# Optimization experiments

Hardware: AMD Instinct MI355X
Metric: run time of the kernel (lower is better)

Reference implementation:

```python
import jax, jax.numpy as jnp
import numpy as np

D = 1024
H = 16
HD = D // H
FF = 4 * D
EPS = 1e-5


def setup_inputs() -> dict:
    key = jax.random.key(0)
    ks = jax.random.split(key, 16)
    s = lambda k, shape, scale: jax.random.normal(k, shape, dtype=jnp.float32) * scale
    inp = {
        "x": s(ks[0], (8, 1024, D), 1.0),
        "Wq": s(ks[1], (D, D), D ** -0.5), "bq": jnp.zeros((D,), jnp.float32),
        "Wk": s(ks[2], (D, D), D ** -0.5), "bk": jnp.zeros((D,), jnp.float32),
        "Wv": s(ks[3], (D, D), D ** -0.5), "bv": jnp.zeros((D,), jnp.float32),
        "Wo": s(ks[4], (D, D), D ** -0.5), "bo": jnp.zeros((D,), jnp.float32),
        "W1": s(ks[5], (D, FF), D ** -0.5), "b1": jnp.zeros((FF,), jnp.float32),
        "W2": s(ks[6], (FF, D), FF ** -0.5), "b2": jnp.zeros((D,), jnp.float32),
        "g1": jnp.ones((D,), jnp.float32), "be1": jnp.zeros((D,), jnp.float32),
        "g2": jnp.ones((D,), jnp.float32), "be2": jnp.zeros((D,), jnp.float32),
    }
    return inp


def _layernorm(x, g, b):
    mu = jnp.mean(x, axis=-1, keepdims=True)
    var = jnp.var(x, axis=-1, keepdims=True)
    return (x - mu) * jax.lax.rsqrt(var + EPS) * g + b


def reference(x, Wq, bq, Wk, bk, Wv, bv, Wo, bo, W1, b1, W2, b2, g1, be1, g2, be2):
    B, S, _ = x.shape
    # --- pre-norm attention block (dropout = identity in eval) ---
    h = _layernorm(x, g1, be1)
    q = (h @ Wq + bq).reshape(B, S, H, HD)
    k = (h @ Wk + bk).reshape(B, S, H, HD)
    v = (h @ Wv + bv).reshape(B, S, H, HD)
    scores = jnp.einsum('bqhd,bkhd->bhqk', q, k) / jnp.sqrt(jnp.float32(HD))
    attn = jax.nn.softmax(scores, axis=-1)
    ctx = jnp.einsum('bhqk,bkhd->bqhd', attn, v).reshape(B, S, D)
    x = x + (ctx @ Wo + bo)
    # --- pre-norm FFN block ---
    h = _layernorm(x, g2, be2)
    h = jax.nn.gelu(h @ W1 + b1, approximate=False)
    x = x + (h @ W2 + b2)
    return x
```

## Files before the change

### kernel.cpp

```cpp
#include <hip/hip_runtime.h>
#include <hip/hip_bf16.h>
#include <math.h>
#include <stdint.h>

typedef unsigned short u16;
typedef unsigned int u32;
typedef __attribute__((ext_vector_type(8))) short short8;
typedef __attribute__((ext_vector_type(4))) float f32x4;

__device__ __forceinline__ float b2f(u16 u) {
  union { u32 i; float f; } v; v.i = ((u32)u) << 16; return v.f;
}
__device__ __forceinline__ u16 f2b(float f) {
  union { float f; u32 i; } v; v.f = f;
  return (u16)((v.i + 0x7FFFu + ((v.i >> 16) & 1u)) >> 16);
}

__device__ __forceinline__ void gload_lds16(const u16* g, u16* l) {
  __builtin_amdgcn_global_load_lds((const __attribute__((address_space(1))) void*)g,
                                   (__attribute__((address_space(3))) void*)l, 16, 0, 0);
}

__global__ __launch_bounds__(256) void transpose_k(const float* __restrict__ in,
                                                   u16* __restrict__ out, int K, int N) {
  __shared__ u16 tile[32][33];
  int n0 = blockIdx.x * 32, k0 = blockIdx.y * 32;
  int tx = threadIdx.x & 31, ty = threadIdx.x >> 5;
  #pragma unroll
  for (int i = ty; i < 32; i += 8)
    tile[i][tx] = f2b(in[(size_t)(k0 + i) * N + n0 + tx]);
  __syncthreads();
  #pragma unroll
  for (int i = ty; i < 32; i += 8)
    out[(size_t)(n0 + i) * K + k0 + tx] = tile[tx][i];
}

__global__ __launch_bounds__(256) void vtrans_k(const u16* __restrict__ v, u16* __restrict__ vt) {
  __shared__ u16 tile[32][33];
  int bh = blockIdx.y, b = bh >> 4, h = bh & 15;
  int s0 = (blockIdx.x & 31) * 32, d0 = (blockIdx.x >> 5) * 32;
  int tx = threadIdx.x & 31, ty = threadIdx.x >> 5;
  #pragma unroll
  for (int i = ty; i < 32; i += 8)
    tile[i][tx] = v[(size_t)(b * 1024 + s0 + i) * 1024 + h * 64 + d0 + tx];
  __syncthreads();
  #pragma unroll
  for (int i = ty; i < 32; i += 8)
    vt[(size_t)(bh * 64 + d0 + i) * 1024 + s0 + tx] = tile[tx][i];
}

template<int FP32IN>
__global__ __launch_bounds__(256) void ln_k(const void* __restrict__ xv, const float* __restrict__ g,
                                            const float* __restrict__ be, u16* __restrict__ out) {
  int row = blockIdx.x, t = threadIdx.x;
  float f0, f1, f2, f3;
  if (FP32IN) {
    const float* xr = (const float*)xv + (size_t)row * 1024;
    float4 x4 = *(const float4*)(xr + t * 4);
    f0 = x4.x; f1 = x4.y; f2 = x4.z; f3 = x4.w;
  } else {
    const u16* xr = (const u16*)xv + (size_t)row * 1024;
    ushort4 x4 = *(const ushort4*)(xr + t * 4);
    f0 = b2f(x4.x); f1 = b2f(x4.y); f2 = b2f(x4.z); f3 = b2f(x4.w);
  }
  float s = f0 + f1 + f2 + f3;
  float ss = f0 * f0 + f1 * f1 + f2 * f2 + f3 * f3;
  #pragma unroll
  for (int off = 32; off > 0; off >>= 1) { s += __shfl_down(s, off); ss += __shfl_down(ss, off); }
  __shared__ float sb[4], ssb[4];
  if ((t & 63) == 0) { sb[t >> 6] = s; ssb[t >> 6] = ss; }
  __syncthreads();
  s = sb[0] + sb[1] + sb[2] + sb[3];
  ss = ssb[0] + ssb[1] + ssb[2] + ssb[3];
  float mu = s * (1.0f / 1024.0f);
  float var = ss * (1.0f / 1024.0f) - mu * mu;
  float rstd = rsqrtf(var + 1e-5f);
  float4 gv = *(const float4*)(g + t * 4);
  float4 bv = *(const float4*)(be + t * 4);
  ushort4 o;
  o.x = f2b((f0 - mu) * rstd * gv.x + bv.x);
  o.y = f2b((f1 - mu) * rstd * gv.y + bv.y);
  o.z = f2b((f2 - mu) * rstd * gv.z + bv.z);
  o.w = f2b((f3 - mu) * rstd * gv.w + bv.w);
  *(ushort4*)(out + (size_t)row * 1024 + t * 4) = o;
}

template<int ACT, int RESID, int OUTF32>
__global__ __launch_bounds__(256) void gemm_k(const u16* __restrict__ A, const u16* __restrict__ Bt,
                                              const float* __restrict__ bias, const void* __restrict__ resid,
                                              void* __restrict__ Cv, int M, int N, int K) {
  __shared__ u16 As[128 * 64];
  __shared__ u16 Bs[128 * 64];
  int n0 = blockIdx.x * 128, m0 = blockIdx.y * 128;
  int t = threadIdx.x;
  int wave = t >> 6, lane = t & 63, quad = lane >> 4, l16 = lane & 15;
  int wm = (wave >> 1) * 64, wn = (wave & 1) * 64;
  f32x4 acc[4][4] = {};
  int lrow = (lane >> 3) & 7;
  int lchunk = (lane & 7) ^ lrow;
  const u16* Ab = A + (size_t)(m0 + wave * 8 + lrow) * K + lchunk * 8;
  const u16* Bb = Bt + (size_t)(n0 + wave * 8 + lrow) * K + lchunk * 8;
  u16* AsW = As + wave * 512;
  u16* BsW = Bs + wave * 512;
  for (int k0 = 0; k0 < K; k0 += 64) {
    #pragma unroll
    for (int it = 0; it < 4; it++) {
      gload_lds16(Ab + k0 + (size_t)it * 32 * K, AsW + it * 2048);
      gload_lds16(Bb + k0 + (size_t)it * 32 * K, BsW + it * 2048);
    }
    __syncthreads();
    #pragma unroll
    for (int kh = 0; kh < 2; kh++) {
      short8 a[4], b[4];
      #pragma unroll
      for (int i = 0; i < 4; i++) {
        int row = wm + i * 16 + l16;
        int pc = (kh * 4 + quad) ^ (row & 7);
        a[i] = *(const short8*)(As + row * 64 + pc * 8);
      }
      #pragma unroll
      for (int j = 0; j < 4; j++) {
        int row = wn + j * 16 + l16;
        int pc = (kh * 4 + quad) ^ (row & 7);
        b[j] = *(const short8*)(Bs + row * 64 + pc * 8);
      }
      #pragma unroll
      for (int i = 0; i < 4; i++)
        #pragma unroll
        for (int j = 0; j < 4; j++)
          acc[i][j] = __builtin_amdgcn_mfma_f32_16x16x32_bf16(a[i], b[j], acc[i][j], 0, 0, 0);
    }
    __syncthreads();
  }
  float bcol[4];
  #pragma unroll
  for (int j = 0; j < 4; j++) bcol[j] = bias[n0 + wn + j * 16 + l16];
  #pragma unroll
  for (int i = 0; i < 4; i++) {
    #pragma unroll
    for (int r = 0; r < 4; r++) {
      int row = m0 + wm + i * 16 + quad * 4 + r;
      #pragma unroll
      for (int j = 0; j < 4; j++) {
        int col = n0 + wn + j * 16 + l16;
        float v = acc[i][j][r] + bcol[j];
        if (ACT == 1) v = 0.5f * v * (1.0f + erff(v * 0.70710678118f));
        if (RESID == 1) v += b2f(((const u16*)resid)[(size_t)row * N + col]);
        if (RESID == 2) v += ((const float*)resid)[(size_t)row * N + col];
        if (OUTF32) ((float*)Cv)[(size_t)row * N + col] = v;
        else        ((u16*)Cv)[(size_t)row * N + col] = f2b(v);
      }
    }
  }
}

__global__ __launch_bounds__(256) void attn_k(const u16* __restrict__ Q, const u16* __restrict__ Kb,
                                              const u16* __restrict__ VT, u16* __restrict__ ctx) {
  int bh = blockIdx.x;
  int b = bh >> 4;
  int q0 = blockIdx.y * 64;
  int t = threadIdx.x, wave = t >> 6, lane = t & 63, quad = lane >> 4, l16 = lane & 15;
  __shared__ u16 Ks[2][64 * 64];
  __shared__ u16 Vs[2][64 * 64];
  __shared__ u16 Plds[4][16][72];
  const size_t base = ((size_t)b * 1024) * 1024 + (size_t)(bh & 15) * 64;
  const u16* Kbase = Kb + base;
  const u16* vtb = VT + (size_t)bh * 64 * 1024;
  int lrow = lane >> 3;
  int lchunk = (lane & 7) ^ (lrow & 7);
  int srow = wave * 16;
  short8 qa[2];
  #pragma unroll
  for (int kh = 0; kh < 2; kh++)
    qa[kh] = *(const short8*)(Q + base + (size_t)(q0 + wave * 16 + l16) * 1024 + kh * 32 + quad * 8);
  #pragma unroll
  for (int half = 0; half < 2; half++) {
    int r8 = srow + half * 8;
    gload_lds16(Kbase + (size_t)(r8 + lrow) * 1024 + lchunk * 8, &Ks[0][r8 * 64]);
    gload_lds16(vtb + (size_t)(r8 + lrow) * 1024 + lchunk * 8, &Vs[0][r8 * 64]);
  }
  f32x4 o[4] = {};
  float l_acc[4] = {0.f, 0.f, 0.f, 0.f};
  for (int c = 0; c < 16; c++) {
    int buf = c & 1;
    __syncthreads();
    if (c < 15) {
      #pragma unroll
      for (int half = 0; half < 2; half++) {
        int r8 = srow + half * 8;
        gload_lds16(Kbase + (size_t)((c + 1) * 64 + r8 + lrow) * 1024 + lchunk * 8, &Ks[buf ^ 1][r8 * 64]);
        gload_lds16(vtb + (size_t)(r8 + lrow) * 1024 + (c + 1) * 64 + lchunk * 8, &Vs[buf ^ 1][r8 * 64]);
      }
    }
    f32x4 s[4] = {};
    #pragma unroll
    for (int kh = 0; kh < 2; kh++)
      #pragma unroll
      for (int j = 0; j < 4; j++) {
        int row = j * 16 + l16;
        int pc = (kh * 4 + quad) ^ (row & 7);
        short8 kb = *(const short8*)(&Ks[buf][row * 64 + pc * 8]);
        s[j] = __builtin_amdgcn_mfma_f32_16x16x32_bf16(qa[kh], kb, s[j], 0, 0, 0);
      }
    #pragma unroll
    for (int j = 0; j < 4; j++)
      #pragma unroll
      for (int r = 0; r < 4; r++) {
        float p = exp2f(s[j][r] * 0.18033688011112042f);
        l_acc[r] += p;
        Plds[wave][quad * 4 + r][j * 16 + l16] = f2b(p);
      }
    #pragma unroll
    for (int kh = 0; kh < 2; kh++) {
      short8 pa = *(const short8*)(&Plds[wave][l16][kh * 32 + quad * 8]);
      #pragma unroll
      for (int d4 = 0; d4 < 4; d4++) {
        int row = d4 * 16 + l16;
        int pc = (kh * 4 + quad) ^ (row & 7);
        short8 vb = *(const short8*)(&Vs[buf][row * 64 + pc * 8]);
        o[d4] = __builtin_amdgcn_mfma_f32_16x16x32_bf16(pa, vb, o[d4], 0, 0, 0);
      }
    }
  }
  #pragma unroll
  for (int off = 1; off < 16; off <<= 1)
    #pragma unroll
    for (int r = 0; r < 4; r++) l_acc[r] += __shfl_xor(l_acc[r], off);
  #pragma unroll
  for (int r = 0; r < 4; r++) {
    float inv = 1.0f / l_acc[r];
    size_t row = (size_t)b * 1024 + q0 + wave * 16 + quad * 4 + r;
    #pragma unroll
    for (int d4 = 0; d4 < 4; d4++) {
      int col = (bh & 15) * 64 + d4 * 16 + l16;
      ctx[row * 1024 + col] = f2b(o[d4][r] * inv);
    }
  }
}

extern "C" void kernel_launch(void* const* d_in, const int* in_sizes, int n_in,
                              void* d_out, int out_size, void* d_ws, size_t ws_size,
                              hipStream_t stream) {
  const float* x   = (const float*)d_in[0];
  const float* Wq  = (const float*)d_in[1];  const float* bq  = (const float*)d_in[2];
  const float* Wk  = (const float*)d_in[3];  const float* bk  = (const float*)d_in[4];
  const float* Wv  = (const float*)d_in[5];  const float* bv  = (const float*)d_in[6];
  const float* Wo  = (const float*)d_in[7];  const float* bo  = (const float*)d_in[8];
  const float* W1  = (const float*)d_in[9];  const float* b1  = (const float*)d_in[10];
  const float* W2  = (const float*)d_in[11]; const float* b2  = (const float*)d_in[12];
  const float* g1  = (const float*)d_in[13]; const float* be1 = (const float*)d_in[14];
  const float* g2  = (const float*)d_in[15]; const float* be2 = (const float*)d_in[16];

  char* ws = (char*)d_ws;
  const size_t MB = 1024 * 1024;
  const bool full = ws_size >= 144 * MB;
  u16* R0  = (u16*)(ws + 0 * MB);
  u16* R1  = (u16*)(ws + 16 * MB);
  u16* R2  = (u16*)(ws + 32 * MB);
  u16* WqT = (u16*)(ws + 48 * MB);
  u16* WkT = (u16*)(ws + 50 * MB);
  u16* WvT = (u16*)(ws + 52 * MB);
  u16* WoT = (u16*)(ws + 54 * MB);
  u16* W1T = full ? (u16*)(ws + 64 * MB) : (u16*)(ws + 56 * MB);
  u16* W2T = full ? (u16*)(ws + 72 * MB) : R2;
  u16* h3f = (u16*)(ws + 80 * MB);
  float* out = (float*)d_out;
  u16* vb  = (u16*)d_out;
  u16* ctx = (u16*)d_out;
  u16* h2  = full ? R2 : (u16*)d_out + (size_t)8192 * 1024;
  u16* vt  = R0;

  transpose_k<<<dim3(32, 32), 256, 0, stream>>>(Wq, WqT, 1024, 1024);
  transpose_k<<<dim3(32, 32), 256, 0, stream>>>(Wk, WkT, 1024, 1024);
  transpose_k<<<dim3(32, 32), 256, 0, stream>>>(Wv, WvT, 1024, 1024);
  transpose_k<<<dim3(32, 32), 256, 0, stream>>>(Wo, WoT, 1024, 1024);
  transpose_k<<<dim3(128, 32), 256, 0, stream>>>(W1, W1T, 1024, 4096);
  if (full) transpose_k<<<dim3(32, 128), 256, 0, stream>>>(W2, W2T, 4096, 1024);

  ln_k<1><<<8192, 256, 0, stream>>>(x, g1, be1, R0);

  gemm_k<0, 0, 0><<<dim3(8, 64), 256, 0, stream>>>(R0, WqT, bq, nullptr, R1, 8192, 1024, 1024);
  gemm_k<0, 0, 0><<<dim3(8, 64), 256, 0, stream>>>(R0, WkT, bk, nullptr, R2, 8192, 1024, 1024);
  gemm_k<0, 0, 0><<<dim3(8, 64), 256, 0, stream>>>(R0, WvT, bv, nullptr, vb, 8192, 1024, 1024);

  vtrans_k<<<dim3(64, 128), 256, 0, stream>>>(vb, vt);

  attn_k<<<dim3(128, 16), 256, 0, stream>>>(R1, R2, vt, ctx);

  gemm_k<0, 2, 0><<<dim3(8, 64), 256, 0, stream>>>(ctx, WoT, bo, x, R1, 8192, 1024, 1024);

  if (!full) transpose_k<<<dim3(32, 128), 256, 0, stream>>>(W2, W2T, 4096, 1024);

  ln_k<0><<<8192, 256, 0, stream>>>(R1, g2, be2, h2);

  if (full) {
    gemm_k<1, 0, 0><<<dim3(32, 64), 256, 0, stream>>>(h2, W1T, b1, nullptr, h3f, 8192, 4096, 1024);
    gemm_k<0, 1, 1><<<dim3(8, 64), 256, 0, stream>>>(h3f, W2T, b2, R1, out, 8192, 1024, 4096);
  } else {
    for (int m = 0; m < 4; m++) {
      const u16* h2c = h2 + (size_t)m * 2048 * 1024;
      const u16* x1c = R1 + (size_t)m * 2048 * 1024;
      float* outc = out + (size_t)m * 2048 * 1024;
      gemm_k<1, 0, 0><<<dim3(32, 16), 256, 0, stream>>>(h2c, W1T, b1, nullptr, R0, 2048, 4096, 1024);
      gemm_k<0, 1, 1><<<dim3(8, 16), 256, 0, stream>>>(R0, W2T, b2, x1c, outc, 2048, 1024, 4096);
    }
  }

  (void)in_sizes; (void)n_in; (void)out_size; (void)ws_size;
}
```

Before: 568.4 us.

## Double-buffer GEMM K-tiles in LDS and use exp-based tanh GELU

```diff
diff --git a/kernel.cpp b/kernel.cpp
--- a/kernel.cpp
+++ b/kernel.cpp
@@ -89,48 +89,48 @@
 __global__ __launch_bounds__(256) void gemm_k(const u16* __restrict__ A, const u16* __restrict__ Bt,
                                               const float* __restrict__ bias, const void* __restrict__ resid,
                                               void* __restrict__ Cv, int M, int N, int K) {
-  __shared__ u16 As[128 * 64];
-  __shared__ u16 Bs[128 * 64];
+  __shared__ u16 As[2][128 * 32];
+  __shared__ u16 Bs[2][128 * 32];
   int n0 = blockIdx.x * 128, m0 = blockIdx.y * 128;
   int t = threadIdx.x;
   int wave = t >> 6, lane = t & 63, quad = lane >> 4, l16 = lane & 15;
   int wm = (wave >> 1) * 64, wn = (wave & 1) * 64;
   f32x4 acc[4][4] = {};
-  int lrow = (lane >> 3) & 7;
-  int lchunk = (lane & 7) ^ lrow;
-  const u16* Ab = A + (size_t)(m0 + wave * 8 + lrow) * K + lchunk * 8;
-  const u16* Bb = Bt + (size_t)(n0 + wave * 8 + lrow) * K + lchunk * 8;
-  u16* AsW = As + wave * 512;
-  u16* BsW = Bs + wave * 512;
-  for (int k0 = 0; k0 < K; k0 += 64) {
-    #pragma unroll
-    for (int it = 0; it < 4; it++) {
-      gload_lds16(Ab + k0 + (size_t)it * 32 * K, AsW + it * 2048);
-      gload_lds16(Bb + k0 + (size_t)it * 32 * K, BsW + it * 2048);
-    }
+  int lr = lane >> 2;
+  int lc = (lane & 3) ^ (lr & 3);
+  const u16* Ab = A + (size_t)(m0 + wave * 16 + lr) * K + lc * 8;
+  const u16* Bb = Bt + (size_t)(n0 + wave * 16 + lr) * K + lc * 8;
+  const int lb = wave * 16 * 32;
+  const int rdoff = (quad ^ (l16 & 3)) * 8;
+  #pragma unroll
+  for (int i = 0; i < 2; i++) {
+    gload_lds16(Ab + (size_t)i * 64 * K, &As[0][lb + i * 64 * 32]);
+    gload_lds16(Bb + (size_t)i * 64 * K, &Bs[0][lb + i * 64 * 32]);
+  }
+  const int niter = K >> 5;
+  for (int c = 0; c < niter; c++) {
+    int buf = c & 1;
     __syncthreads();
-    #pragma unroll
-    for (int kh = 0; kh < 2; kh++) {
-      short8 a[4], b[4];
-      #pragma unroll
-      for (int i = 0; i < 4; i++) {
-        int row = wm + i * 16 + l16;
-        int pc = (kh * 4 + quad) ^ (row & 7);
-        a[i] = *(const short8*)(As + row * 64 + pc * 8);
-      }
-      #pragma unroll
-      for (int j = 0; j < 4; j++) {
-        int row = wn + j * 16 + l16;
-        int pc = (kh * 4 + quad) ^ (row & 7);
-        b[j] = *(const short8*)(Bs + row * 64 + pc * 8);
-      }
-      #pragma unroll
-      for (int i = 0; i < 4; i++)
-        #pragma unroll
-        for (int j = 0; j < 4; j++)
-          acc[i][j] = __builtin_amdgcn_mfma_f32_16x16x32_bf16(a[i], b[j], acc[i][j], 0, 0, 0);
-    }
-    __syncthreads();
+    if (c + 1 < niter) {
+      int k1 = (c + 1) << 5;
+      #pragma unroll
+      for (int i = 0; i < 2; i++) {
+        gload_lds16(Ab + k1 + (size_t)i * 64 * K, &As[buf ^ 1][lb + i * 64 * 32]);
+        gload_lds16(Bb + k1 + (size_t)i * 64 * K, &Bs[buf ^ 1][lb + i * 64 * 32]);
+      }
+    }
+    short8 a[4], b[4];
+    #pragma unroll
+    for (int i = 0; i < 4; i++)
+      a[i] = *(const short8*)(&As[buf][(wm + i * 16 + l16) * 32 + rdoff]);
+    #pragma unroll
+    for (int j = 0; j < 4; j++)
+      b[j] = *(const short8*)(&Bs[buf][(wn + j * 16 + l16) * 32 + rdoff]);
+    #pragma unroll
+    for (int i = 0; i < 4; i++)
+      #pragma unroll
+      for (int j = 0; j < 4; j++)
+        acc[i][j] = __builtin_amdgcn_mfma_f32_16x16x32_bf16(a[i], b[j], acc[i][j], 0, 0, 0);
   }
   float bcol[4];
   #pragma unroll
@@ -144,7 +144,11 @@
       for (int j = 0; j < 4; j++) {
         int col = n0 + wn + j * 16 + l16;
         float v = acc[i][j][r] + bcol[j];
-        if (ACT == 1) v = 0.5f * v * (1.0f + erff(v * 0.70710678118f));
+        if (ACT == 1) {
+          float e = v * (2.3022082f + 0.1029431f * v * v);
+          float tt = exp2f(fminf(e, 80.0f));
+          v = v * tt / (tt + 1.0f);
+        }
         if (RESID == 1) v += b2f(((const u16*)resid)[(size_t)row * N + col]);
         if (RESID == 2) v += ((const float*)resid)[(size_t)row * N + col];
         if (OUTF32) ((float*)Cv)[(size_t)row * N + col] = v;
```

New measurement: 576.3 us. About the same (+1.4%).
